# Performance work log

Measured on AMD Instinct MI355X. Metric: run time of the kernel, lower is better.

Reference implementation:

```python
import jax, jax.numpy as jnp
import numpy as np

N = 100_000   # nodes
E = 3_200_000 # edges
B = 64        # graphs in batch
OUT = 64      # config


def setup_inputs() -> dict:
    key = jax.random.key(0)
    ks = jax.random.split(key, 12)
    x = jax.random.normal(ks[0], (N, 3), dtype=jnp.float32)
    edge_index = jax.random.randint(ks[1], (2, E), 0, N, dtype=jnp.int32)
    batch = jnp.sort(jax.random.randint(ks[2], (N,), 0, B, dtype=jnp.int32))
    # GCNConv weights (PyG: out = norm_adj @ (x @ W) + b)
    W1 = jax.random.normal(ks[3], (3, 32), dtype=jnp.float32) * 0.5
    b1 = jnp.zeros((32,), dtype=jnp.float32)
    W2 = jax.random.normal(ks[4], (32, 32), dtype=jnp.float32) * 0.18
    b2 = jnp.zeros((32,), dtype=jnp.float32)
    LW1 = jax.random.normal(ks[5], (64, 64), dtype=jnp.float32) * 0.125
    Lb1 = jnp.zeros((64,), dtype=jnp.float32)
    LW2 = jax.random.normal(ks[6], (64, OUT), dtype=jnp.float32) * 0.125
    Lb2 = jnp.zeros((OUT,), dtype=jnp.float32)
    return {"x": x, "edge_index": edge_index, "batch": batch,
            "W1": W1, "b1": b1, "W2": W2, "b2": b2,
            "LW1": LW1, "Lb1": Lb1, "LW2": LW2, "Lb2": Lb2}


def _gcn_norm(edge_index, n):
    # add self-loops, compute symmetric normalization D^-1/2 (A+I) D^-1/2
    loops = jnp.arange(n, dtype=edge_index.dtype)
    src = jnp.concatenate([edge_index[0], loops])
    dst = jnp.concatenate([edge_index[1], loops])
    deg = jax.ops.segment_sum(jnp.ones_like(dst, dtype=jnp.float32), dst,
                              num_segments=n)
    dinv = jnp.where(deg > 0, 1.0 / jnp.sqrt(deg), 0.0)
    norm = dinv[src] * dinv[dst]  # [E+N]
    return src, dst, norm


def _gcn_conv(x, W, b, src, dst, norm, n):
    h = x @ W                         # [N, F_out] tiny GEMM
    m = h[src] * norm[:, None]        # edge gather  [E+N, F_out]
    out = jax.ops.segment_sum(m, dst, num_segments=n)  # scatter-add
    return out + b


def _pool(x, batch, nb):
    # cat(global_max_pool, global_mean_pool)
    mx = jax.ops.segment_max(x, batch, num_segments=nb)
    sm = jax.ops.segment_sum(x, batch, num_segments=nb)
    cnt = jax.ops.segment_sum(jnp.ones((x.shape[0],), x.dtype), batch,
                              num_segments=nb)
    mean = sm / jnp.maximum(cnt, 1.0)[:, None]
    return jnp.concatenate([mx, mean], axis=1)


def reference(x, edge_index, batch, W1, b1, W2, b2, LW1, Lb1, LW2, Lb2):
    n = x.shape[0]
    src, dst, norm = _gcn_norm(edge_index, n)
    h = jax.nn.relu(_gcn_conv(x, W1, b1, src, dst, norm, n))
    x1 = _pool(h, batch, B)           # [B, 64]
    h2 = jax.nn.relu(_gcn_conv(h, W2, b2, src, dst, norm, n))
    x2 = _pool(h2, batch, B)          # [B, 64]
    z = jax.nn.relu((x1 + x2) @ LW1 + Lb1)
    # dropout p=0.5 skipped (eval mode / training=False)
    out = z @ LW2 + Lb2               # [B, OUT]; .squeeze(1) is a no-op for OUT>1
    return out
```

## Files before the change

kernel.cpp:

```cpp
#include <hip/hip_runtime.h>
#include <hip/hip_fp16.h>


#define F 32
#define POOLD 64
#define BKT 512
#define BKTL2 9
#define EPB 8192
#define MAXBUCK 256

typedef __attribute__((ext_vector_type(8))) _Float16 half8;

__global__ void k_histB(const int* __restrict__ ei, int* __restrict__ bcnt,
                        int e, int nbuck, int nblk) {
    __shared__ int h[MAXBUCK];
    for (int b = threadIdx.x; b < nbuck; b += 256) h[b] = 0;
    __syncthreads();
    int base = blockIdx.x * EPB;
#pragma unroll
    for (int k = 0; k < EPB / 1024; ++k) {
        int i = base + (k * 256 + threadIdx.x) * 4;
        if (i + 4 <= e) {
            int4 d4 = *reinterpret_cast<const int4*>(ei + e + i);
            atomicAdd(&h[d4.x >> BKTL2], 1);
            atomicAdd(&h[d4.y >> BKTL2], 1);
            atomicAdd(&h[d4.z >> BKTL2], 1);
            atomicAdd(&h[d4.w >> BKTL2], 1);
        } else {
            for (int j = i; j < e && j < i + 4; ++j)
                atomicAdd(&h[ei[e + j] >> BKTL2], 1);
        }
    }
    __syncthreads();
    for (int b = threadIdx.x; b < nbuck; b += 256)
        bcnt[b * nblk + blockIdx.x] = h[b];
}

__global__ void k_rowscan(int* __restrict__ bcnt, int* __restrict__ tot, int nblk) {
    __shared__ int lds[256];
    int* row = bcnt + (size_t)blockIdx.x * nblk;
    int t = threadIdx.x;
    int running = 0;
    for (int chunk = 0; chunk < nblk; chunk += 256) {
        int idx = chunk + t;
        int v = (idx < nblk) ? row[idx] : 0;
        lds[t] = v;
        __syncthreads();
        int val = v;
        for (int off = 1; off < 256; off <<= 1) {
            int other = (t >= off) ? lds[t - off] : 0;
            __syncthreads();
            val += other;
            lds[t] = val;
            __syncthreads();
        }
        if (idx < nblk) row[idx] = running + val - v;
        running += lds[255];
        __syncthreads();
    }
    if (t == 0) tot[blockIdx.x] = running;
}

__global__ void k_bscan(const int* __restrict__ tot, int* __restrict__ bstart,
                        int nbuck, int e) {
    __shared__ int lds[256];
    int t = threadIdx.x;
    int v = (t < nbuck) ? tot[t] : 0;
    lds[t] = v;
    __syncthreads();
    int val = v;
    for (int off = 1; off < 256; off <<= 1) {
        int other = (t >= off) ? lds[t - off] : 0;
        __syncthreads();
        val += other;
        lds[t] = val;
        __syncthreads();
    }
    if (t < nbuck) bstart[t] = val - v;
    if (t == 0) bstart[nbuck] = e;
}

__global__ void k_bin(const int* __restrict__ ei, const int* __restrict__ bstart,
                      const int* __restrict__ bcnt, int* __restrict__ packed,
                      int e, int nbuck, int nblk) {
    __shared__ int cur[MAXBUCK];
    for (int b = threadIdx.x; b < nbuck; b += 256)
        cur[b] = bstart[b] + bcnt[b * nblk + blockIdx.x];
    __syncthreads();
    int base = blockIdx.x * EPB;
#pragma unroll
    for (int k = 0; k < EPB / 1024; ++k) {
        int i = base + (k * 256 + threadIdx.x) * 4;
        if (i + 4 <= e) {
            int4 s4 = *reinterpret_cast<const int4*>(ei + i);
            int4 d4 = *reinterpret_cast<const int4*>(ei + e + i);
            int p0 = atomicAdd(&cur[d4.x >> BKTL2], 1);
            int p1 = atomicAdd(&cur[d4.y >> BKTL2], 1);
            int p2 = atomicAdd(&cur[d4.z >> BKTL2], 1);
            int p3 = atomicAdd(&cur[d4.w >> BKTL2], 1);
            packed[p0] = (s4.x << BKTL2) | (d4.x & (BKT - 1));
            packed[p1] = (s4.y << BKTL2) | (d4.y & (BKT - 1));
            packed[p2] = (s4.z << BKTL2) | (d4.z & (BKT - 1));
            packed[p3] = (s4.w << BKTL2) | (d4.w & (BKT - 1));
        } else {
            for (int j = i; j < e && j < i + 4; ++j) {
                int s = ei[j], d = ei[e + j];
                int p = atomicAdd(&cur[d >> BKTL2], 1);
                packed[p] = (s << BKTL2) | (d & (BKT - 1));
            }
        }
    }
}

__global__ void k_place2(const int* __restrict__ packed, const int* __restrict__ bstart,
                         int* __restrict__ col, int* __restrict__ rp,
                         float* __restrict__ dinv, int n) {
    __shared__ int deg[BKT];
    __shared__ int sc[BKT];
    __shared__ int cur[BKT];
    int t = threadIdx.x;
    deg[t] = 0;
    __syncthreads();
    int start = bstart[blockIdx.x];
    int end = bstart[blockIdx.x + 1];
    for (int i = start + t; i < end; i += BKT)
        atomicAdd(&deg[packed[i] & (BKT - 1)], 1);
    __syncthreads();
    int d0 = deg[t];
    sc[t] = d0;
    __syncthreads();
    int val = d0;
    for (int off = 1; off < BKT; off <<= 1) {
        int other = (t >= off) ? sc[t - off] : 0;
        __syncthreads();
        val += other;
        sc[t] = val;
        __syncthreads();
    }
    int node = blockIdx.x * BKT + t;
    int ex = start + val - d0;
    if (node < n) {
        rp[node] = ex;
        dinv[node] = rsqrtf((float)d0 + 1.0f);
    }
    cur[t] = ex;
    __syncthreads();
    for (int i = start + t; i < end; i += BKT) {
        int u = packed[i];
        int p = atomicAdd(&cur[u & (BKT - 1)], 1);
        col[p] = u >> BKTL2;
    }
}

__global__ void k_xw1(const float* __restrict__ x, const float* __restrict__ W1,
                      _Float16* __restrict__ h0, int n) {
    int i = blockIdx.x * blockDim.x + threadIdx.x;
    if (i >= n * F) return;
    int node = i >> 5, f = i & (F - 1);
    float x0 = x[node * 3 + 0], x1 = x[node * 3 + 1], x2 = x[node * 3 + 2];
    h0[i] = (_Float16)(x0 * W1[f] + x1 * W1[F + f] + x2 * W1[2 * F + f]);
}

__global__ void k_gemm2(const _Float16* __restrict__ h, const float* __restrict__ W2,
                        _Float16* __restrict__ g, int n) {
    int i = blockIdx.x * blockDim.x + threadIdx.x;
    if (i >= n * F) return;
    int node = i >> 5, f = i & (F - 1);
    const _Float16* row = h + (size_t)node * F;
    float acc = 0.0f;
#pragma unroll
    for (int k = 0; k < F; ++k) acc += (float)row[k] * W2[k * F + f];
    g[i] = (_Float16)acc;
}

__global__ void k_gather(const _Float16* __restrict__ hin, const int* __restrict__ rp,
                         const int* __restrict__ col, const float* __restrict__ dinv,
                         const float* __restrict__ bias, const int* __restrict__ batch,
                         _Float16* __restrict__ hout,
                         float* __restrict__ psum, float* __restrict__ pmax,
                         float* __restrict__ cnt, int n, int ne, int store, int do_cnt) {
    int t = blockIdx.x * blockDim.x + threadIdx.x;
    int node = t >> 2, q = t & 3;
    if (node >= n) return;
    int start = rp[node];
    int end = (node + 1 < n) ? rp[node + 1] : ne;
    float dv = dinv[node];

    half8 hv = *reinterpret_cast<const half8*>(hin + (size_t)node * F + q * 8);
    float dvv = dv * dv;
    float acc[8];
#pragma unroll
    for (int j = 0; j < 8; ++j) acc[j] = (float)hv[j] * dvv;

    int e = start;
    for (; e + 4 <= end; e += 4) {
        int s0 = col[e + 0], s1 = col[e + 1], s2 = col[e + 2], s3 = col[e + 3];
        float w0 = dinv[s0] * dv, w1 = dinv[s1] * dv,
              w2 = dinv[s2] * dv, w3 = dinv[s3] * dv;
        half8 v0 = *reinterpret_cast<const half8*>(hin + (size_t)s0 * F + q * 8);
        half8 v1 = *reinterpret_cast<const half8*>(hin + (size_t)s1 * F + q * 8);
        half8 v2 = *reinterpret_cast<const half8*>(hin + (size_t)s2 * F + q * 8);
        half8 v3 = *reinterpret_cast<const half8*>(hin + (size_t)s3 * F + q * 8);
#pragma unroll
        for (int j = 0; j < 8; ++j)
            acc[j] += (float)v0[j] * w0 + (float)v1[j] * w1 +
                      (float)v2[j] * w2 + (float)v3[j] * w3;
    }
    for (; e < end; ++e) {
        int s = col[e];
        float wv = dinv[s] * dv;
        half8 v = *reinterpret_cast<const half8*>(hin + (size_t)s * F + q * 8);
#pragma unroll
        for (int j = 0; j < 8; ++j) acc[j] += (float)v[j] * wv;
    }

    float vv[8];
#pragma unroll
    for (int j = 0; j < 8; ++j) vv[j] = fmaxf(acc[j] + bias[q * 8 + j], 0.0f);
    if (store) {
        half8 o;
#pragma unroll
        for (int j = 0; j < 8; ++j) o[j] = (_Float16)vv[j];
        *reinterpret_cast<half8*>(hout + (size_t)node * F + q * 8) = o;
    }

    int b = batch[node];
    int lane = threadIdx.x & 63;
    int bFirst = __shfl(b, 0);
    int bLast  = __shfl(b, 63);
    if (bFirst == bLast) {
        float sv[8], mv[8];
#pragma unroll
        for (int j = 0; j < 8; ++j) { sv[j] = vv[j]; mv[j] = vv[j]; }
        for (int off = 4; off < 64; off <<= 1) {
#pragma unroll
            for (int j = 0; j < 8; ++j) {
                sv[j] += __shfl_down(sv[j], off);
                mv[j] = fmaxf(mv[j], __shfl_down(mv[j], off));
            }
        }
        if (lane < 4) {
            float* ps = psum + b * F + lane * 8;
            int* pm = reinterpret_cast<int*>(pmax + b * F + lane * 8);
#pragma unroll
            for (int j = 0; j < 8; ++j) {
                atomicAdd(ps + j, sv[j]);
                atomicMax(pm + j, __float_as_int(mv[j]));
            }
            if (do_cnt && lane == 0) atomicAdd(&cnt[b], 16.0f);
        }
    } else {
        float* ps = psum + b * F + q * 8;
        int* pm = reinterpret_cast<int*>(pmax + b * F + q * 8);
#pragma unroll
        for (int j = 0; j < 8; ++j) {
            atomicAdd(ps + j, vv[j]);
            atomicMax(pm + j, __float_as_int(vv[j]));
        }
        if (do_cnt && q == 0) atomicAdd(&cnt[b], 1.0f);
    }
}

__global__ void k_mlp(const float* __restrict__ sum1, const float* __restrict__ max1,
                      const float* __restrict__ sum2, const float* __restrict__ max2,
                      const float* __restrict__ cnt,
                      const float* __restrict__ LW1, const float* __restrict__ Lb1,
                      const float* __restrict__ LW2, const float* __restrict__ Lb2,
                      float* __restrict__ out, int outd) {
    __shared__ float zs[POOLD];
    int b = blockIdx.x, j = threadIdx.x;
    float invc = 1.0f / fmaxf(cnt[b], 1.0f);
    float acc = Lb1[j];
#pragma unroll
    for (int i = 0; i < POOLD; ++i) {
        float s;
        if (i < F) s = max1[b * F + i] + max2[b * F + i];
        else       s = (sum1[b * F + i - F] + sum2[b * F + i - F]) * invc;
        acc += s * LW1[i * POOLD + j];
    }
    zs[j] = fmaxf(acc, 0.0f);
    __syncthreads();
    if (j < outd) {
        float a2 = Lb2[j];
#pragma unroll
        for (int jj = 0; jj < POOLD; ++jj) a2 += zs[jj] * LW2[jj * outd + j];
        out[b * outd + j] = a2;
    }
}

extern "C" void kernel_launch(void* const* d_in, const int* in_sizes, int n_in,
                              void* d_out, int out_size, void* d_ws, size_t ws_size,
                              hipStream_t stream) {
    const float* x    = (const float*)d_in[0];
    const int*   ei   = (const int*)d_in[1];
    const int*   batch= (const int*)d_in[2];
    const float* W1   = (const float*)d_in[3];
    const float* b1   = (const float*)d_in[4];
    const float* W2   = (const float*)d_in[5];
    const float* b2   = (const float*)d_in[6];
    const float* LW1  = (const float*)d_in[7];
    const float* Lb1  = (const float*)d_in[8];
    const float* LW2  = (const float*)d_in[9];
    const float* Lb2  = (const float*)d_in[10];
    float* out = (float*)d_out;

    const int N = in_sizes[0] / 3;
    const int E = in_sizes[1] / 2;
    const int OUTD = in_sizes[10];
    const int B = out_size / OUTD;
    const int poolsz = 4 * B * F + B;
    const int NBUCK = (N + BKT - 1) / BKT;
    const int NBLK = (E + EPB - 1) / EPB;

    char* p = (char*)d_ws;
    float* pools= (float*)p;          p += (size_t)poolsz * 4;
    int* bcnt   = (int*)p;            p += (size_t)NBUCK * NBLK * 4;
    int* tot    = (int*)p;            p += (size_t)MAXBUCK * 4;
    int* bstart = (int*)p;            p += (size_t)(NBUCK + 1) * 4;
    int* rowptr = (int*)p;            p += (size_t)N * 4;
    int* col    = (int*)p;            p += (size_t)E * 4;
    float* dinv = (float*)p;          p += (size_t)N * 4;
    _Float16* buf0 = (_Float16*)p;    p += (size_t)N * F * 2;
    _Float16* buf1 = (_Float16*)p;    p += (size_t)N * F * 2;
    int* packed = (int*)buf0;
    float* sum1 = pools;
    float* max1 = sum1 + B * F;
    float* sum2 = max1 + B * F;
    float* max2 = sum2 + B * F;
    float* cnt  = max2 + B * F;

    const int BS = 256;
    auto g1 = [&](long long n) { return (int)((n + BS - 1) / BS); };

    hipMemsetAsync(pools, 0, (size_t)poolsz * 4, stream);
    k_histB<<<NBLK, BS, 0, stream>>>(ei, bcnt, E, NBUCK, NBLK);
    k_rowscan<<<NBUCK, 256, 0, stream>>>(bcnt, tot, NBLK);
    k_bscan<<<1, 256, 0, stream>>>(tot, bstart, NBUCK, E);
    k_bin<<<NBLK, BS, 0, stream>>>(ei, bstart, bcnt, packed, E, NBUCK, NBLK);
    k_place2<<<NBUCK, BKT, 0, stream>>>(packed, bstart, col, rowptr, dinv, N);

    k_xw1<<<g1((long long)N * F), BS, 0, stream>>>(x, W1, buf0, N);
    k_gather<<<g1((long long)N * 4), BS, 0, stream>>>(buf0, rowptr, col, dinv, b1,
                                                      batch, buf1, sum1, max1, cnt,
                                                      N, E, 1, 1);
    k_gemm2<<<g1((long long)N * F), BS, 0, stream>>>(buf1, W2, buf0, N);
    k_gather<<<g1((long long)N * 4), BS, 0, stream>>>(buf0, rowptr, col, dinv, b2,
                                                      batch, buf1, sum2, max2, cnt,
                                                      N, E, 0, 0);

    k_mlp<<<B, 64, 0, stream>>>(sum1, max1, sum2, max2, cnt,
                                LW1, Lb1, LW2, Lb2, out, OUTD);
}
```

Baseline: 342.1 us.

## Split feature matrices into two 16-wide half planes and gather each separately

Stores node features as two planes of 16 halves (32 bytes per node) instead of one 64-byte row, and runs the neighbour gather twice per layer, once per plane, with 2 threads per node and an 8-way unrolled edge loop. The aim is to halve the working set of each gather pass (3.2 MB per plane) so random neighbour reads hit cache better. In exchange, CSR indices and dinv are read twice per layer and there are more kernel launches.

```diff
diff --git a/kernel.cpp b/kernel.cpp
--- a/kernel.cpp
+++ b/kernel.cpp
@@ -153,75 +153,87 @@
 }
 
 __global__ void k_xw1(const float* __restrict__ x, const float* __restrict__ W1,
-                      _Float16* __restrict__ h0, int n) {
+                      _Float16* __restrict__ p0, _Float16* __restrict__ p1, int n) {
     int i = blockIdx.x * blockDim.x + threadIdx.x;
     if (i >= n * F) return;
     int node = i >> 5, f = i & (F - 1);
     float x0 = x[node * 3 + 0], x1 = x[node * 3 + 1], x2 = x[node * 3 + 2];
-    h0[i] = (_Float16)(x0 * W1[f] + x1 * W1[F + f] + x2 * W1[2 * F + f]);
-}
-
-__global__ void k_gemm2(const _Float16* __restrict__ h, const float* __restrict__ W2,
-                        _Float16* __restrict__ g, int n) {
+    float v = x0 * W1[f] + x1 * W1[F + f] + x2 * W1[2 * F + f];
+    _Float16* plane = (f < 16) ? p0 : p1;
+    plane[node * 16 + (f & 15)] = (_Float16)v;
+}
+
+__global__ void k_gemm2(const _Float16* __restrict__ h0, const _Float16* __restrict__ h1,
+                        const float* __restrict__ W2,
+                        _Float16* __restrict__ g0, _Float16* __restrict__ g1, int n) {
     int i = blockIdx.x * blockDim.x + threadIdx.x;
     if (i >= n * F) return;
     int node = i >> 5, f = i & (F - 1);
-    const _Float16* row = h + (size_t)node * F;
+    const _Float16* r0 = h0 + (size_t)node * 16;
+    const _Float16* r1 = h1 + (size_t)node * 16;
     float acc = 0.0f;
 #pragma unroll
-    for (int k = 0; k < F; ++k) acc += (float)row[k] * W2[k * F + f];
-    g[i] = (_Float16)acc;
-}
-
-__global__ void k_gather(const _Float16* __restrict__ hin, const int* __restrict__ rp,
+    for (int k = 0; k < 16; ++k) acc += (float)r0[k] * W2[k * F + f];
+#pragma unroll
+    for (int k = 0; k < 16; ++k) acc += (float)r1[k] * W2[(k + 16) * F + f];
+    _Float16* plane = (f < 16) ? g0 : g1;
+    plane[node * 16 + (f & 15)] = (_Float16)acc;
+}
+
+__global__ void k_gather(const _Float16* __restrict__ plane, const int* __restrict__ rp,
                          const int* __restrict__ col, const float* __restrict__ dinv,
                          const float* __restrict__ bias, const int* __restrict__ batch,
-                         _Float16* __restrict__ hout,
+                         _Float16* __restrict__ outPlane,
                          float* __restrict__ psum, float* __restrict__ pmax,
-                         float* __restrict__ cnt, int n, int ne, int store, int do_cnt) {
+                         float* __restrict__ cnt, int n, int ne, int fh,
+                         int store, int do_cnt) {
     int t = blockIdx.x * blockDim.x + threadIdx.x;
-    int node = t >> 2, q = t & 3;
+    int node = t >> 1, q = t & 1;
     if (node >= n) return;
     int start = rp[node];
     int end = (node + 1 < n) ? rp[node + 1] : ne;
     float dv = dinv[node];
 
-    half8 hv = *reinterpret_cast<const half8*>(hin + (size_t)node * F + q * 8);
+    half8 hv = *reinterpret_cast<const half8*>(plane + (size_t)node * 16 + q * 8);
     float dvv = dv * dv;
     float acc[8];
 #pragma unroll
     for (int j = 0; j < 8; ++j) acc[j] = (float)hv[j] * dvv;
 
     int e = start;
-    for (; e + 4 <= end; e += 4) {
-        int s0 = col[e + 0], s1 = col[e + 1], s2 = col[e + 2], s3 = col[e + 3];
-        float w0 = dinv[s0] * dv, w1 = dinv[s1] * dv,
-              w2 = dinv[s2] * dv, w3 = dinv[s3] * dv;
-        half8 v0 = *reinterpret_cast<const half8*>(hin + (size_t)s0 * F + q * 8);
-        half8 v1 = *reinterpret_cast<const half8*>(hin + (size_t)s1 * F + q * 8);
-        half8 v2 = *reinterpret_cast<const half8*>(hin + (size_t)s2 * F + q * 8);
-        half8 v3 = *reinterpret_cast<const half8*>(hin + (size_t)s3 * F + q * 8);
-#pragma unroll
-        for (int j = 0; j < 8; ++j)
-            acc[j] += (float)v0[j] * w0 + (float)v1[j] * w1 +
-                      (float)v2[j] * w2 + (float)v3[j] * w3;
+    for (; e + 8 <= end; e += 8) {
+        int s[8];
+#pragma unroll
+        for (int u = 0; u < 8; ++u) s[u] = col[e + u];
+        half8 v[8];
+#pragma unroll
+        for (int u = 0; u < 8; ++u)
+            v[u] = *reinterpret_cast<const half8*>(plane + (size_t)s[u] * 16 + q * 8);
+        float w[8];
+#pragma unroll
+        for (int u = 0; u < 8; ++u) w[u] = dinv[s[u]] * dv;
+#pragma unroll
+        for (int u = 0; u < 8; ++u)
+#pragma unroll
+            for (int j = 0; j < 8; ++j) acc[j] += (float)v[u][j] * w[u];
     }
     for (; e < end; ++e) {
         int s = col[e];
         float wv = dinv[s] * dv;
-        half8 v = *reinterpret_cast<const half8*>(hin + (size_t)s * F + q * 8);
+        half8 v = *reinterpret_cast<const half8*>(plane + (size_t)s * 16 + q * 8);
 #pragma unroll
         for (int j = 0; j < 8; ++j) acc[j] += (float)v[j] * wv;
     }
 
     float vv[8];
 #pragma unroll
-    for (int j = 0; j < 8; ++j) vv[j] = fmaxf(acc[j] + bias[q * 8 + j], 0.0f);
+    for (int j = 0; j < 8; ++j)
+        vv[j] = fmaxf(acc[j] + bias[fh * 16 + q * 8 + j], 0.0f);
     if (store) {
         half8 o;
 #pragma unroll
         for (int j = 0; j < 8; ++j) o[j] = (_Float16)vv[j];
-        *reinterpret_cast<half8*>(hout + (size_t)node * F + q * 8) = o;
+        *reinterpret_cast<half8*>(outPlane + (size_t)node * 16 + q * 8) = o;
     }
 
     int b = batch[node];
@@ -232,26 +244,26 @@
         float sv[8], mv[8];
 #pragma unroll
         for (int j = 0; j < 8; ++j) { sv[j] = vv[j]; mv[j] = vv[j]; }
-        for (int off = 4; off < 64; off <<= 1) {
+        for (int off = 2; off < 64; off <<= 1) {
 #pragma unroll
             for (int j = 0; j < 8; ++j) {
                 sv[j] += __shfl_down(sv[j], off);
                 mv[j] = fmaxf(mv[j], __shfl_down(mv[j], off));
             }
         }
-        if (lane < 4) {
-            float* ps = psum + b * F + lane * 8;
-            int* pm = reinterpret_cast<int*>(pmax + b * F + lane * 8);
+        if (lane < 2) {
+            float* ps = psum + b * F + fh * 16 + lane * 8;
+            int* pm = reinterpret_cast<int*>(pmax + b * F + fh * 16 + lane * 8);
 #pragma unroll
             for (int j = 0; j < 8; ++j) {
                 atomicAdd(ps + j, sv[j]);
                 atomicMax(pm + j, __float_as_int(mv[j]));
             }
-            if (do_cnt && lane == 0) atomicAdd(&cnt[b], 16.0f);
+            if (do_cnt && lane == 0) atomicAdd(&cnt[b], 32.0f);
         }
     } else {
-        float* ps = psum + b * F + q * 8;
-        int* pm = reinterpret_cast<int*>(pmax + b * F + q * 8);
+        float* ps = psum + b * F + fh * 16 + q * 8;
+        int* pm = reinterpret_cast<int*>(pmax + b * F + fh * 16 + q * 8);
 #pragma unroll
         for (int j = 0; j < 8; ++j) {
             atomicAdd(ps + j, vv[j]);
@@ -320,9 +332,11 @@
     int* rowptr = (int*)p;            p += (size_t)N * 4;
     int* col    = (int*)p;            p += (size_t)E * 4;
     float* dinv = (float*)p;          p += (size_t)N * 4;
-    _Float16* buf0 = (_Float16*)p;    p += (size_t)N * F * 2;
-    _Float16* buf1 = (_Float16*)p;    p += (size_t)N * F * 2;
-    int* packed = (int*)buf0;
+    _Float16* b0p0 = (_Float16*)p;    p += (size_t)N * 16 * 2;
+    _Float16* b0p1 = (_Float16*)p;    p += (size_t)N * 16 * 2;
+    _Float16* b1p0 = (_Float16*)p;    p += (size_t)N * 16 * 2;
+    _Float16* b1p1 = (_Float16*)p;    p += (size_t)N * 16 * 2;
+    int* packed = (int*)b0p0;
     float* sum1 = pools;
     float* max1 = sum1 + B * F;
     float* sum2 = max1 + B * F;
@@ -339,14 +353,20 @@
     k_bin<<<NBLK, BS, 0, stream>>>(ei, bstart, bcnt, packed, E, NBUCK, NBLK);
     k_place2<<<NBUCK, BKT, 0, stream>>>(packed, bstart, col, rowptr, dinv, N);
 
-    k_xw1<<<g1((long long)N * F), BS, 0, stream>>>(x, W1, buf0, N);
-    k_gather<<<g1((long long)N * 4), BS, 0, stream>>>(buf0, rowptr, col, dinv, b1,
-                                                      batch, buf1, sum1, max1, cnt,
-                                                      N, E, 1, 1);
-    k_gemm2<<<g1((long long)N * F), BS, 0, stream>>>(buf1, W2, buf0, N);
-    k_gather<<<g1((long long)N * 4), BS, 0, stream>>>(buf0, rowptr, col, dinv, b2,
-                                                      batch, buf1, sum2, max2, cnt,
-                                                      N, E, 0, 0);
+    k_xw1<<<g1((long long)N * F), BS, 0, stream>>>(x, W1, b0p0, b0p1, N);
+    k_gather<<<g1((long long)N * 2), BS, 0, stream>>>(b0p0, rowptr, col, dinv, b1,
+                                                      batch, b1p0, sum1, max1, cnt,
+                                                      N, E, 0, 1, 1);
+    k_gather<<<g1((long long)N * 2), BS, 0, stream>>>(b0p1, rowptr, col, dinv, b1,
+                                                      batch, b1p1, sum1, max1, cnt,
+                                                      N, E, 1, 1, 0);
+    k_gemm2<<<g1((long long)N * F), BS, 0, stream>>>(b1p0, b1p1, W2, b0p0, b0p1, N);
+    k_gather<<<g1((long long)N * 2), BS, 0, stream>>>(b0p0, rowptr, col, dinv, b2,
+                                                      batch, b1p0, sum2, max2, cnt,
+                                                      N, E, 0, 0, 0);
+    k_gather<<<g1((long long)N * 2), BS, 0, stream>>>(b0p1, rowptr, col, dinv, b2,
+                                                      batch, b1p1, sum2, max2, cnt,
+                                                      N, E, 1, 0, 0);
 
     k_mlp<<<B, 64, 0, stream>>>(sum1, max1, sum2, max2, cnt,
                                 LW1, Lb1, LW2, Lb2, out, OUTD);
```

After: 389.8 us. 1.14x slower.
